# Performance work log

Hardware: AMD Instinct MI355X
Metric: run time of the kernel (lower is better)

Reference implementation:

```python
import jax, jax.numpy as jnp
import numpy as np

T, X_D, M_N, CHUNK, REDUCE = 2048, 2048, 64, 64, 8
M_D = X_D // REDUCE          # 256
DECAY_D = M_D // 4           # 64
H_D = X_D * 2                # factor=2
FF_D = 256 * round(int(H_D * (2.0 / 3.0)) / 256)  # 2816


def setup_inputs() -> dict:
    key = jax.random.key(0)
    ks = jax.random.split(key, 20)
    def lin(k, out_d, in_d):
        return (jax.random.normal(k, (out_d, in_d), jnp.float32) / np.sqrt(in_d).astype(np.float32))
    return {
        "xs": jax.random.normal(ks[0], (T, X_D), jnp.float32),
        "attn_q": lin(ks[1], X_D // REDUCE, X_D),
        "attn_k": lin(ks[2], X_D // REDUCE, X_D // REDUCE),
        "attn_v": lin(ks[3], X_D, X_D),
        "attn_o": lin(ks[4], X_D, X_D),
        "attn_r": lin(ks[5], X_D, X_D),
        "mem_f": lin(ks[6], M_N, X_D),
        "mem_q": lin(ks[7], M_D, X_D),
        "mem_k": lin(ks[8], M_D, M_D),
        "mem_v": lin(ks[9], M_D, X_D),
        "mem_o": lin(ks[10], X_D, M_D),
        "mem_r": lin(ks[11], X_D, X_D),
        "mem_beta": -jnp.ones((M_N, M_D), jnp.float32),
        "mem_decay": 3.0 * jnp.ones((M_N, DECAY_D), jnp.float32),
        "mem_l": jax.random.uniform(ks[12], (M_N, M_D), dtype=jnp.float32),
        "ff_in1": lin(ks[13], FF_D, X_D),
        "ff_in2": lin(ks[14], FF_D, X_D),
        "ff_out": lin(ks[15], X_D, FF_D),
        "sn1_g": jnp.sqrt(jnp.float32(X_D)),
        "sn2_g": jnp.sqrt(jnp.float32(X_D)),
    }


def _rotate_half(x):
    x1 = x[..., ::2]
    x2 = x[..., 1::2]
    return jnp.stack((-x2, x1), axis=-1).reshape(x.shape)


def _scale_norm(x, g):
    return x * (g / (jnp.linalg.norm(x, axis=-1, keepdims=True) + 1e-8))


def _attn(xs, Wq, Wk, Wv, Wo, Wr):
    n = CHUNK
    q = xs @ Wq.T                       # (T, dk)
    k = q @ Wk.T                        # k is computed from q (as in source)
    v = xs @ Wv.T                       # (T, x_d)
    c = xs.shape[0] // n
    dk = q.shape[-1]
    q = q.reshape(c, n, dk)
    k = k.reshape(c, n, dk)
    v = v.reshape(c, n, v.shape[-1])

    def with_prev(a):                   # prepend previous chunk (zero for chunk 0)
        prev = jnp.concatenate([jnp.zeros_like(a[:1]), a[:-1]], axis=0)
        return jnp.concatenate([prev, a], axis=1)   # (c, 2n, d)

    k2, v2 = with_prev(k), with_prev(v)

    # RoPE over 2n key positions; queries take the last n positions
    inv_freq = 1.0 / (10000.0 ** (jnp.arange(0, dk, 2, dtype=jnp.float32) / dk))
    ang = jnp.arange(2 * n, dtype=jnp.float32)[:, None] * inv_freq[None, :]
    sin = jnp.repeat(jnp.sin(ang), 2, axis=-1)      # (2n, dk) interleaved
    cos = jnp.repeat(jnp.cos(ang), 2, axis=-1)
    q = q * cos[None, n:] + _rotate_half(q) * sin[None, n:]
    k2 = k2 * cos[None] + _rotate_half(k2) * sin[None]

    qk = jnp.einsum('cnk,cmk->cnm', q, k2) / jnp.sqrt(jnp.float32(dk))
    allowed = jnp.arange(2 * n)[None, :] <= (jnp.arange(n)[:, None] + n)  # tril offset n
    A = jax.nn.softmax(jnp.where(allowed[None], qk, -jnp.inf), axis=-1)
    y = jnp.einsum('cnm,cmv->cnv', A, v2).reshape(xs.shape[0], -1)
    return (y @ Wo.T) * jax.nn.sigmoid(xs @ Wr.T)


def _mem(xs, Wf, Wq, Wk, Wv, Wo, Wr, beta_p, decay_p, l_p):
    v = xs @ Wv.T                                       # (T, m_d)
    f = jax.nn.sigmoid(xs @ Wf.T)[:, :, None]           # (T, m_n, 1)
    beta = jax.nn.sigmoid(beta_p)[None]                 # (1, m_n, m_d)
    gamma = jnp.concatenate(
        [jnp.ones((M_N, M_D - DECAY_D), xs.dtype), jax.nn.sigmoid(decay_p)], axis=1
    )[None]                                             # (1, m_n, m_d)
    ws = (1.0 - f * beta) * gamma                       # (T, m_n, m_d)
    fvs = f * v[:, None, :]                             # (T, m_n, m_d)

    def bin_assoc(ei, ej):
        ai, bi = ei
        aj, bj = ej
        return (aj * ai, aj * bi + bj)

    _, mems = jax.lax.associative_scan(bin_assoc, (ws, fvs), axis=0)  # (T, m_n, m_d)

    q = xs @ Wq.T                                       # (T, m_d)
    k = jnp.einsum('nmd,kd->nmk', mems, Wk) + l_p[None]
    A = jax.nn.softmax(jnp.einsum('nmk,nk->nm', k, q) / jnp.sqrt(jnp.float32(M_D)), axis=-1)
    y = jnp.einsum('nm,nmd->nd', A, mems)
    return (y @ Wo.T) * jax.nn.sigmoid(xs @ Wr.T)


def _ff(xs, W1, W2, Wo):
    return (jax.nn.silu(xs @ W1.T) * (xs @ W2.T)) @ Wo.T


def reference(xs, attn_q, attn_k, attn_v, attn_o, attn_r,
              mem_f, mem_q, mem_k, mem_v, mem_o, mem_r,
              mem_beta, mem_decay, mem_l,
              ff_in1, ff_in2, ff_out, sn1_g, sn2_g):
    xn = _scale_norm(xs, sn1_g)
    xs = (_attn(xn, attn_q, attn_k, attn_v, attn_o, attn_r)
          + _mem(xn, mem_f, mem_q, mem_k, mem_v, mem_o, mem_r, mem_beta, mem_decay, mem_l)
          + xs)
    xs = _ff(_scale_norm(xs, sn2_g), ff_in1, ff_in2, ff_out) + xs
    return xs
```

## Files before the change

kernel.cpp:

```cpp
#include <hip/hip_runtime.h>
#include <math.h>


typedef short bhalf8 __attribute__((ext_vector_type(8)));
typedef float f32x4 __attribute__((ext_vector_type(4)));

#define CC_LD 7168
#define COL_V   0
#define COL_B1  2048
#define COL_B2  4096
#define COL_QB  6144
#define COL_VM  6400
#define COL_QM  6656
#define COL_FG  6912

#define AS1 __attribute__((address_space(1)))
#define AS3 __attribute__((address_space(3)))

__device__ __forceinline__ float sigmoidf_(float x){ return 1.0f/(1.0f+expf(-x)); }

__device__ __forceinline__ unsigned short f2b(float f){
  unsigned u = __float_as_uint(f);
  unsigned r = (u + 0x7fffu + ((u>>16)&1u)) >> 16;
  return (unsigned short)r;
}
__device__ __forceinline__ float b2f(unsigned short h){
  return __uint_as_float(((unsigned)h)<<16);
}

__global__ void k_f2b_all(
    const float* __restrict__ av, const float* __restrict__ ar, const float* __restrict__ mr,
    const float* __restrict__ aq, const float* __restrict__ mv, const float* __restrict__ mq,
    const float* __restrict__ mf, const float* __restrict__ ao, const float* __restrict__ mo,
    const float* __restrict__ f1, const float* __restrict__ f2, const float* __restrict__ fo,
    const float* __restrict__ ak,
    unsigned short* __restrict__ WCAT, unsigned short* __restrict__ AOB,
    unsigned short* __restrict__ MOB, unsigned short* __restrict__ FFW,
    unsigned short* __restrict__ FFOB, unsigned short* __restrict__ AKB){
  int i = blockIdx.x*256 + threadIdx.x;
  const float* s; unsigned short* d; int off;
  if (i < 3571712){
    d = WCAT + (size_t)i*4;
    if      (i < 1048576){ s = av; off = i; }
    else if (i < 2097152){ s = ar; off = i-1048576; }
    else if (i < 3145728){ s = mr; off = i-2097152; }
    else if (i < 3276800){ s = aq; off = i-3145728; }
    else if (i < 3407872){ s = mv; off = i-3276800; }
    else if (i < 3538944){ s = mq; off = i-3407872; }
    else                 { s = mf; off = i-3538944; }
  }
  else if (i < 4620288){ off = i-3571712; s = ao; d = AOB  + (size_t)off*4; }
  else if (i < 4751360){ off = i-4620288; s = mo; d = MOB  + (size_t)off*4; }
  else if (i < 6193152){ off = i-4751360; s = f1;
    int row = off >> 9, c4 = off & 511;
    d = FFW + ((size_t)row*2)*2048 + c4*4; }
  else if (i < 7634944){ off = i-6193152; s = f2;
    int row = off >> 9, c4 = off & 511;
    d = FFW + ((size_t)row*2 + 1)*2048 + c4*4; }
  else if (i < 9076736){ off = i-7634944; s = fo; d = FFOB + (size_t)off*4; }
  else if (i < 9093120){ off = i-9076736; s = ak; d = AKB  + (size_t)off*4; }
  else return;
  float4 v = ((const float4*)s)[off];
  ushort4 o;
  o.x = f2b(v.x); o.y = f2b(v.y); o.z = f2b(v.z); o.w = f2b(v.w);
  *(ushort4*)d = o;
}

__global__ void k_f2bT(const float* __restrict__ s, unsigned short* __restrict__ d){
  int i = blockIdx.x, j = threadIdx.x;
  d[(size_t)j*256 + i] = f2b(s[(size_t)i*256 + j]);
}

__global__ void k_trig(float2* __restrict__ TR){
  int idx = blockIdx.x*256 + threadIdx.x;
  int pos = idx >> 7, j = idx & 127;
  float inv = powf(10000.f, -(float)j/128.f);
  float a = (float)pos * inv;
  TR[idx] = make_float2(cosf(a), sinf(a));
}

__global__ __launch_bounds__(256) void k_scalenorm_b(const float* __restrict__ x,
    const float* __restrict__ g, unsigned short* __restrict__ ob){
  int row = blockIdx.x, tid = threadIdx.x;
  const float* xr = x + (size_t)row*2048;
  float ss = 0.f;
  for (int j = tid; j < 2048; j += 256){ float v = xr[j]; ss += v*v; }
  __shared__ float red[256];
  red[tid] = ss; __syncthreads();
  for (int s = 128; s > 0; s >>= 1){ if (tid < s) red[tid] += red[tid+s]; __syncthreads(); }
  float scale = g[0] / (sqrtf(red[0]) + 1e-8f);
  unsigned short* orow = ob + (size_t)row*2048;
  for (int j4 = tid; j4 < 512; j4 += 256){
    float4 v = *(const float4*)(xr + j4*4);
    ushort4 o;
    o.x = f2b(v.x*scale); o.y = f2b(v.y*scale); o.z = f2b(v.z*scale); o.w = f2b(v.w*scale);
    ((ushort4*)orow)[j4] = o;
  }
}

__global__ __launch_bounds__(256) void k_gemm_p(
    const unsigned short* __restrict__ A, int lda,
    const unsigned short* __restrict__ B,
    float* __restrict__ C, unsigned short* __restrict__ Cb,
    int N, int K, int ldc, int epi,
    const float* __restrict__ add,
    const unsigned short* __restrict__ gate, int gate_ld,
    const unsigned short* A2, const unsigned short* B2, float* C2){
  __shared__ unsigned short LDSu[24576];
  int tid = threadIdx.x;
  int w = tid >> 6, l = tid & 63;
  int bi = blockIdx.y, bj = blockIdx.x;
  const unsigned short* Ap = A; const unsigned short* Bp = B; float* Cp = C;
  if (blockIdx.z){ Ap = A2; Bp = B2; Cp = C2; }
  int m0 = bi*128, n0 = bj*128;
  int wr = w >> 1, wc = w & 1;

  f32x4 acc[4][4];
#pragma unroll
  for (int i=0;i<4;++i)
#pragma unroll
    for (int j=0;j<4;++j){ f32x4 z = {0.f,0.f,0.f,0.f}; acc[i][j] = z; }

  const int r0 = tid >> 2;
  const int gsrc8 = (((tid&3) ^ ((tid>>3)&3)) * 8);

  auto stage = [&](int bs, int kt){
    unsigned short* db = LDSu + bs*8192;
    const unsigned short* ap0 = Ap + (size_t)(m0 + r0)*lda      + kt*32 + gsrc8;
    const unsigned short* ap1 = Ap + (size_t)(m0 + 64 + r0)*lda + kt*32 + gsrc8;
    const unsigned short* bp0 = Bp + (size_t)(n0 + r0)*K        + kt*32 + gsrc8;
    const unsigned short* bp1 = Bp + (size_t)(n0 + 64 + r0)*K   + kt*32 + gsrc8;
    __builtin_amdgcn_global_load_lds((const AS1 void*)ap0, (AS3 void*)(db + tid*8),        16, 0, 0);
    __builtin_amdgcn_global_load_lds((const AS1 void*)ap1, (AS3 void*)(db + 2048 + tid*8), 16, 0, 0);
    __builtin_amdgcn_global_load_lds((const AS1 void*)bp0, (AS3 void*)(db + 4096 + tid*8), 16, 0, 0);
    __builtin_amdgcn_global_load_lds((const AS1 void*)bp1, (AS3 void*)(db + 6144 + tid*8), 16, 0, 0);
  };

  const int nt = K >> 5;
  stage(0, 0);
  stage(1, 1);
  asm volatile("s_waitcnt vmcnt(4)" ::: "memory");
  __builtin_amdgcn_s_barrier();

  const int lr = l & 15;
  const int gsw = (((l>>4) ^ ((l>>1)&3)) * 8);
  const int aoff = (wr*64 + lr)*32 + gsw;
  const int boff = 4096 + (wc*64 + lr)*32 + gsw;

  int cur = 0;
  for (int t = 0; t < nt; ++t){
    if (t + 2 < nt) stage((t+2)%3, t+2);
    const unsigned short* Tb = LDSu + cur*8192;
    bhalf8 af[4], bfr[4];
#pragma unroll
    for (int m=0;m<4;++m) af[m]  = *(const bhalf8*)(Tb + aoff + m*512);
#pragma unroll
    for (int n=0;n<4;++n) bfr[n] = *(const bhalf8*)(Tb + boff + n*512);
    __builtin_amdgcn_s_setprio(1);
#pragma unroll
    for (int m=0;m<4;++m)
#pragma unroll
      for (int n=0;n<4;++n)
        acc[m][n] = __builtin_amdgcn_mfma_f32_16x16x32_bf16(af[m], bfr[n], acc[m][n], 0, 0, 0);
    __builtin_amdgcn_s_setprio(0);
    if (t + 1 < nt){
      if (t + 2 < nt){ asm volatile("s_waitcnt vmcnt(4)" ::: "memory"); }
      else           { asm volatile("s_waitcnt vmcnt(0)" ::: "memory"); }
      __builtin_amdgcn_s_barrier();
      cur = (cur == 2) ? 0 : cur + 1;
    }
  }

#pragma unroll
  for (int m=0;m<4;++m){
    int rowb = m0 + wr*64 + m*16 + ((l>>4)<<2);
#pragma unroll
    for (int r=0;r<4;++r){
      int row = rowb + r;
      size_t rbase = (size_t)row*ldc;
      size_t gbase = (size_t)row*gate_ld;
#pragma unroll
      for (int n=0;n<4;++n){
        int col = n0 + wc*64 + n*16 + (l&15);
        float v = acc[m][n][r];
        if (add) v += add[rbase + col];
        if (epi == 2) v *= sigmoidf_(b2f(gate[gbase + col]));
        if (epi == 3) Cb[rbase + col] = f2b(v);
        else          Cp[rbase + col] = v;
      }
    }
  }
}

__global__ __launch_bounds__(256) void k_gemm_silu(
    const unsigned short* __restrict__ A, int lda,
    const unsigned short* __restrict__ B,
    unsigned short* __restrict__ Cb, int K, int out_ld){
  __shared__ unsigned short LDSu[24576];
  int tid = threadIdx.x;
  int w = tid >> 6, l = tid & 63;
  int bi = blockIdx.y, bj = blockIdx.x;
  int m0 = bi*128, n0 = bj*128;
  int wr = w >> 1, wc = w & 1;

  f32x4 acc[4][4];
#pragma unroll
  for (int i=0;i<4;++i)
#pragma unroll
    for (int j=0;j<4;++j){ f32x4 z = {0.f,0.f,0.f,0.f}; acc[i][j] = z; }

  const int r0 = tid >> 2;
  const int gsrc8 = (((tid&3) ^ ((tid>>3)&3)) * 8);

  auto stage = [&](int bs, int kt){
    unsigned short* db = LDSu + bs*8192;
    const unsigned short* ap0 = A + (size_t)(m0 + r0)*lda      + kt*32 + gsrc8;
    const unsigned short* ap1 = A + (size_t)(m0 + 64 + r0)*lda + kt*32 + gsrc8;
    const unsigned short* bp0 = B + (size_t)(n0 + r0)*K        + kt*32 + gsrc8;
    const unsigned short* bp1 = B + (size_t)(n0 + 64 + r0)*K   + kt*32 + gsrc8;
    __builtin_amdgcn_global_load_lds((const AS1 void*)ap0, (AS3 void*)(db + tid*8),        16, 0, 0);
    __builtin_amdgcn_global_load_lds((const AS1 void*)ap1, (AS3 void*)(db + 2048 + tid*8), 16, 0, 0);
    __builtin_amdgcn_global_load_lds((const AS1 void*)bp0, (AS3 void*)(db + 4096 + tid*8), 16, 0, 0);
    __builtin_amdgcn_global_load_lds((const AS1 void*)bp1, (AS3 void*)(db + 6144 + tid*8), 16, 0, 0);
  };

  const int nt = K >> 5;
  stage(0, 0);
  stage(1, 1);
  asm volatile("s_waitcnt vmcnt(4)" ::: "memory");
  __builtin_amdgcn_s_barrier();

  const int lr = l & 15;
  const int gsw = (((l>>4) ^ ((l>>1)&3)) * 8);
  const int aoff = (wr*64 + lr)*32 + gsw;
  const int boff = 4096 + (wc*64 + lr)*32 + gsw;

  int cur = 0;
  for (int t = 0; t < nt; ++t){
    if (t + 2 < nt) stage((t+2)%3, t+2);
    const unsigned short* Tb = LDSu + cur*8192;
    bhalf8 af[4], bfr[4];
#pragma unroll
    for (int m=0;m<4;++m) af[m]  = *(const bhalf8*)(Tb + aoff + m*512);
#pragma unroll
    for (int n=0;n<4;++n) bfr[n] = *(const bhalf8*)(Tb + boff + n*512);
    __builtin_amdgcn_s_setprio(1);
#pragma unroll
    for (int m=0;m<4;++m)
#pragma unroll
      for (int n=0;n<4;++n)
        acc[m][n] = __builtin_amdgcn_mfma_f32_16x16x32_bf16(af[m], bfr[n], acc[m][n], 0, 0, 0);
    __builtin_amdgcn_s_setprio(0);
    if (t + 1 < nt){
      if (t + 2 < nt){ asm volatile("s_waitcnt vmcnt(4)" ::: "memory"); }
      else           { asm volatile("s_waitcnt vmcnt(0)" ::: "memory"); }
      __builtin_amdgcn_s_barrier();
      cur = (cur == 2) ? 0 : cur + 1;
    }
  }

#pragma unroll
  for (int m=0;m<4;++m){
    int rowb = m0 + wr*64 + m*16 + ((l>>4)<<2);
#pragma unroll
    for (int r=0;r<4;++r){
      int row = rowb + r;
      size_t gbase = (size_t)row*out_ld;
#pragma unroll
      for (int n=0;n<4;++n){
        int col = n0 + wc*64 + n*16 + (l&15);
        float v = acc[m][n][r];
        float o = __shfl_xor(v, 1);
        if ((l & 1) == 0)
          Cb[gbase + (col>>1)] = f2b(v*sigmoidf_(v)*o);
      }
    }
  }
}

__global__ __launch_bounds__(256) void k_gemm_fuse2(
    const unsigned short* __restrict__ A,  const unsigned short* __restrict__ B,
    const unsigned short* __restrict__ A2, const unsigned short* __restrict__ B2,
    const unsigned short* __restrict__ gate1, const unsigned short* __restrict__ gate2,
    const float* __restrict__ xs, float* __restrict__ XS2){
  __shared__ unsigned short LDSu[24576];
  int tid = threadIdx.x;
  int w = tid >> 6, l = tid & 63;
  int bi = blockIdx.y, bj = blockIdx.x;
  int m0 = bi*128, n0 = bj*128;
  int wr = w >> 1, wc = w & 1;

  f32x4 acc[4][4], acc2[4][4];
#pragma unroll
  for (int i=0;i<4;++i)
#pragma unroll
    for (int j=0;j<4;++j){ f32x4 z = {0.f,0.f,0.f,0.f}; acc[i][j] = z; acc2[i][j] = z; }

  const int r0 = tid >> 2;
  const int gsrc8 = (((tid&3) ^ ((tid>>3)&3)) * 8);

  auto stage = [&](int bs, int kt, const unsigned short* Ap, int lda,
                   const unsigned short* Bp, int ldb){
    unsigned short* db = LDSu + bs*8192;
    const unsigned short* ap0 = Ap + (size_t)(m0 + r0)*lda      + kt*32 + gsrc8;
    const unsigned short* ap1 = Ap + (size_t)(m0 + 64 + r0)*lda + kt*32 + gsrc8;
    const unsigned short* bp0 = Bp + (size_t)(n0 + r0)*ldb      + kt*32 + gsrc8;
    const unsigned short* bp1 = Bp + (size_t)(n0 + 64 + r0)*ldb + kt*32 + gsrc8;
    __builtin_amdgcn_global_load_lds((const AS1 void*)ap0, (AS3 void*)(db + tid*8),        16, 0, 0);
    __builtin_amdgcn_global_load_lds((const AS1 void*)ap1, (AS3 void*)(db + 2048 + tid*8), 16, 0, 0);
    __builtin_amdgcn_global_load_lds((const AS1 void*)bp0, (AS3 void*)(db + 4096 + tid*8), 16, 0, 0);
    __builtin_amdgcn_global_load_lds((const AS1 void*)bp1, (AS3 void*)(db + 6144 + tid*8), 16, 0, 0);
  };

  const int lr = l & 15;
  const int gsw = (((l>>4) ^ ((l>>1)&3)) * 8);
  const int aoff = (wr*64 + lr)*32 + gsw;
  const int boff = 4096 + (wc*64 + lr)*32 + gsw;

  {
    const int nt = 64;
    stage(0, 0, A, 2048, B, 2048);
    stage(1, 1, A, 2048, B, 2048);
    asm volatile("s_waitcnt vmcnt(4)" ::: "memory");
    __builtin_amdgcn_s_barrier();
    int cur = 0;
    for (int t = 0; t < nt; ++t){
      if (t + 2 < nt) stage((t+2)%3, t+2, A, 2048, B, 2048);
      const unsigned short* Tb = LDSu + cur*8192;
      bhalf8 af[4], bfr[4];
#pragma unroll
      for (int m=0;m<4;++m) af[m]  = *(const bhalf8*)(Tb + aoff + m*512);
#pragma unroll
      for (int n=0;n<4;++n) bfr[n] = *(const bhalf8*)(Tb + boff + n*512);
      __builtin_amdgcn_s_setprio(1);
#pragma unroll
      for (int m=0;m<4;++m)
#pragma unroll
        for (int n=0;n<4;++n)
          acc[m][n] = __builtin_amdgcn_mfma_f32_16x16x32_bf16(af[m], bfr[n], acc[m][n], 0, 0, 0);
      __builtin_amdgcn_s_setprio(0);
      if (t + 1 < nt){
        if (t + 2 < nt){ asm volatile("s_waitcnt vmcnt(4)" ::: "memory"); }
        else           { asm volatile("s_waitcnt vmcnt(0)" ::: "memory"); }
        __builtin_amdgcn_s_barrier();
        cur = (cur == 2) ? 0 : cur + 1;
      }
    }
  }
  __syncthreads();

  {
    const int nt = 8;
    stage(0, 0, A2, 256, B2, 256);
    stage(1, 1, A2, 256, B2, 256);
    asm volatile("s_waitcnt vmcnt(4)" ::: "memory");
    __builtin_amdgcn_s_barrier();
    int cur = 0;
    for (int t = 0; t < nt; ++t){
      if (t + 2 < nt) stage((t+2)%3, t+2, A2, 256, B2, 256);
      const unsigned short* Tb = LDSu + cur*8192;
      bhalf8 af[4], bfr[4];
#pragma unroll
      for (int m=0;m<4;++m) af[m]  = *(const bhalf8*)(Tb + aoff + m*512);
#pragma unroll
      for (int n=0;n<4;++n) bfr[n] = *(const bhalf8*)(Tb + boff + n*512);
      __builtin_amdgcn_s_setprio(1);
#pragma unroll
      for (int m=0;m<4;++m)
#pragma unroll
        for (int n=0;n<4;++n)
          acc2[m][n] = __builtin_amdgcn_mfma_f32_16x16x32_bf16(af[m], bfr[n], acc2[m][n], 0, 0, 0);
      __builtin_amdgcn_s_setprio(0);
      if (t + 1 < nt){
        if (t + 2 < nt){ asm volatile("s_waitcnt vmcnt(4)" ::: "memory"); }
        else           { asm volatile("s_waitcnt vmcnt(0)" ::: "memory"); }
        __builtin_amdgcn_s_barrier();
        cur = (cur == 2) ? 0 : cur + 1;
      }
    }
  }

#pragma unroll
  for (int m=0;m<4;++m){
    int rowb = m0 + wr*64 + m*16 + ((l>>4)<<2);
#pragma unroll
    for (int r=0;r<4;++r){
      int row = rowb + r;
      size_t gb = (size_t)row*CC_LD;
      size_t rb = (size_t)row*2048;
#pragma unroll
      for (int n=0;n<4;++n){
        int col = n0 + wc*64 + n*16 + (l&15);
        float v = acc[m][n][r]*sigmoidf_(b2f(gate1[gb + col]))
                + acc2[m][n][r]*sigmoidf_(b2f(gate2[gb + col]))
                + xs[rb + col];
        XS2[rb + col] = v;
      }
    }
  }
}

__global__ __launch_bounds__(256) void k_attn_scores_mfma(
    const unsigned short* __restrict__ CCqb, const float* __restrict__ K0,
    const float2* __restrict__ TR, unsigned short* __restrict__ P){
  __shared__ unsigned short Ks[128*256];
  int c = blockIdx.x, tid = threadIdx.x;
  for (int it = 0; it < 16; ++it){
    int id = tid + it*256;
    int m = id >> 5;
    int cs = (id & 31) * 8;
    float v[8];
    if (c == 0 && m < 64){
#pragma unroll
      for (int u=0;u<8;++u) v[u] = 0.f;
    } else {
      int gr = (c-1)*64 + m;
      const float* kr = K0 + (size_t)gr*256 + cs;
      float4 x0 = *(const float4*)kr, x1 = *(const float4*)(kr+4);
      v[0]=x0.x; v[1]=x0.y; v[2]=x0.z; v[3]=x0.w;
      v[4]=x1.x; v[5]=x1.y; v[6]=x1.z; v[7]=x1.w;
#pragma unroll
      for (int p2=0;p2<4;++p2){
        float2 t = TR[m*128 + (cs>>1) + p2];
        float e = v[2*p2], o = v[2*p2+1];
        v[2*p2]   = e*t.x - o*t.y;
        v[2*p2+1] = o*t.x + e*t.y;
      }
    }
    unsigned short pk[8];
#pragma unroll
    for (int u=0;u<8;++u) pk[u] = f2b(v[u]);
    int byte = m*512 + ((cs*2) ^ ((m&7)<<4));
    *(bhalf8*)((char*)&Ks[0] + byte) = *(const bhalf8*)pk;
  }
  __syncthreads();

  int w = tid >> 6, l = tid & 63;
  int lr = l & 15, lkg = l >> 4;
  f32x4 acc[8];
#pragma unroll
  for (int n=0;n<8;++n){ f32x4 z = {0.f,0.f,0.f,0.f}; acc[n] = z; }

  int iq = w*16 + lr;
  const unsigned short* qbase = CCqb + (size_t)(c*64 + iq)*CC_LD;
  int pos = 64 + iq;

  for (int kt = 0; kt < 8; ++kt){
    int k0c = kt*32 + lkg*8;
    bhalf8 q8 = *(const bhalf8*)(qbase + k0c);
    float v[8];
#pragma unroll
    for (int u=0;u<8;++u) v[u] = b2f((unsigned short)(((short*)&q8)[u]));
#pragma unroll
    for (int p2=0;p2<4;++p2){
      float2 t = TR[pos*128 + (k0c>>1) + p2];
      float e = v[2*p2], o = v[2*p2+1];
      v[2*p2]   = e*t.x - o*t.y;
      v[2*p2+1] = o*t.x + e*t.y;
    }
    unsigned short pk[8];
#pragma unroll
    for (int u=0;u<8;++u) pk[u] = f2b(v[u]);
    bhalf8 af = *(const bhalf8*)pk;
#pragma unroll
    for (int n=0;n<8;++n){
      int m = n*16 + lr;
      int byte = m*512 + ((k0c*2) ^ ((m&7)<<4));
      bhalf8 bf = *(const bhalf8*)((const char*)&Ks[0] + byte);
      acc[n] = __builtin_amdgcn_mfma_f32_16x16x32_bf16(af, bf, acc[n], 0, 0, 0);
    }
  }

  int i0 = w*16 + lkg*4;
  float mx[4] = {-1e30f,-1e30f,-1e30f,-1e30f};
  float sm[4] = {0.f,0.f,0.f,0.f};
#pragma unroll
  for (int n=0;n<8;++n){
    int col = n*16 + lr;
#pragma unroll
    for (int r=0;r<4;++r){
      float vv = acc[n][r] * (1.f/16.f);
      if (col > i0 + r + 64) vv = -1e30f;
      acc[n][r] = vv;
      mx[r] = fmaxf(mx[r], vv);
    }
  }
#pragma unroll
  for (int s=1; s<16; s<<=1)
#pragma unroll
    for (int r=0;r<4;++r) mx[r] = fmaxf(mx[r], __shfl_xor(mx[r], s));
#pragma unroll
  for (int n=0;n<8;++n)
#pragma unroll
    for (int r=0;r<4;++r){
      float e = expf(acc[n][r] - mx[r]);
      acc[n][r] = e; sm[r] += e;
    }
#pragma unroll
  for (int s=1; s<16; s<<=1)
#pragma unroll
    for (int r=0;r<4;++r) sm[r] += __shfl_xor(sm[r], s);
  float rcp[4];
#pragma unroll
  for (int r=0;r<4;++r) rcp[r] = 1.f/sm[r];

  unsigned short* Pr = P + (size_t)c*8192;
#pragma unroll
  for (int n=0;n<8;++n){
    int col = n*16 + lr;
#pragma unroll
    for (int r=0;r<4;++r)
      Pr[(i0+r)*128 + col] = f2b(acc[n][r]*rcp[r]);
  }
}

__global__ __launch_bounds__(256) void k_attn_pv_mfma(
    const unsigned short* __restrict__ P, const unsigned short* __restrict__ Vb, int vld,
    unsigned short* __restrict__ Y){
  __shared__ unsigned short Vt[128*128];
  int ct = blockIdx.x, c = blockIdx.y, tid = threadIdx.x;
  {
    int k = tid >> 1;
    int ch = (tid & 1) * 64;
    if (c == 0 && k < 64){
      for (int u=0; u<64; ++u){
        int col = ch + u;
        int byte = col*256 + ((k*2) ^ ((col&7)<<4));
        *(unsigned short*)((char*)&Vt[0] + byte) = 0;
      }
    } else {
      int gr = (c-1)*64 + k;
      const unsigned short* vr = Vb + (size_t)gr*vld + ct*128 + ch;
      for (int u8=0; u8<8; ++u8){
        bhalf8 x = *(const bhalf8*)(vr + u8*8);
#pragma unroll
        for (int u=0;u<8;++u){
          int col = ch + u8*8 + u;
          int byte = col*256 + ((k*2) ^ ((col&7)<<4));
          *(unsigned short*)((char*)&Vt[0] + byte) = (unsigned short)(((short*)&x)[u]);
        }
      }
    }
  }
  __syncthreads();
  int w = tid >> 6, l = tid & 63, lr = l & 15, lkg = l >> 4;
  f32x4 acc[8];
#pragma unroll
  for (int n=0;n<8;++n){ f32x4 z = {0.f,0.f,0.f,0.f}; acc[n] = z; }
  const unsigned short* Pr = P + (size_t)c*8192;
  for (int kt=0; kt<4; ++kt){
    int kb = kt*32 + lkg*8;
    bhalf8 af = *(const bhalf8*)(Pr + (w*16 + lr)*128 + kb);
#pragma unroll
    for (int n=0;n<8;++n){
      int col = n*16 + lr;
      int byte = col*256 + ((kb*2) ^ ((col&7)<<4));
      bhalf8 bf = *(const bhalf8*)((const char*)&Vt[0] + byte);
      acc[n] = __builtin_amdgcn_mfma_f32_16x16x32_bf16(af, bf, acc[n], 0, 0, 0);
    }
  }
  int row0 = c*64 + w*16 + lkg*4;
#pragma unroll
  for (int n=0;n<8;++n){
    int col = ct*128 + n*16 + lr;
#pragma unroll
    for (int r=0;r<4;++r)
      Y[(size_t)(row0+r)*2048 + col] = f2b(acc[n][r]);
  }
}

__global__ __launch_bounds__(256) void k_scan1(const unsigned short* __restrict__ CC,
    const float* __restrict__ beta_p, const float* __restrict__ decay_p,
    float* __restrict__ CP, float* __restrict__ CQ){
  int c = blockIdx.x, mg = blockIdx.y, d = threadIdx.x;
  __shared__ float Fs[512];
  for (int v = threadIdx.x; v < 512; v += 256){
    int s = v >> 3, j = v & 7;
    Fs[v] = sigmoidf_(b2f(CC[(size_t)(c*64+s)*CC_LD + COL_FG + mg*8 + j]));
  }
  __syncthreads();
  float beta[8], gamma[8], Pa[8], Qa[8];
#pragma unroll
  for (int j=0;j<8;++j){
    int m = mg*8+j;
    beta[j]  = sigmoidf_(beta_p[m*256+d]);
    gamma[j] = (d < 192) ? 1.f : sigmoidf_(decay_p[m*64 + (d-192)]);
    Pa[j] = 1.f; Qa[j] = 0.f;
  }
  for (int s = 0; s < 64; ++s){
    float vm = b2f(CC[(size_t)(c*64+s)*CC_LD + COL_VM + d]);
#pragma unroll
    for (int j=0;j<8;++j){
      float f = Fs[s*8+j];
      float w = (1.f - f*beta[j])*gamma[j];
      Pa[j] *= w;
      Qa[j] = w*Qa[j] + f*vm;
    }
  }
#pragma unroll
  for (int j=0;j<8;++j){
    size_t idx = ((size_t)c*64 + mg*8 + j)*256 + d;
    CP[idx] = Pa[j]; CQ[idx] = Qa[j];
  }
}

__global__ __launch_bounds__(256) void k_scan2(const float* __restrict__ CP,
    const float* __restrict__ CQ, float* __restrict__ SIN){
  int m = blockIdx.x, d = threadIdx.x;
  float S = 0.f;
  for (int c = 0; c < 32; ++c){
    size_t idx = ((size_t)c*64 + m)*256 + d;
    SIN[idx] = S;
    S = CP[idx]*S + CQ[idx];
  }
}

__global__ __launch_bounds__(256) void k_scan3(const unsigned short* __restrict__ CC,
    const float* __restrict__ beta_p, const float* __restrict__ decay_p,
    const float* __restrict__ SIN, unsigned short* __restrict__ MEMS){
  int c = blockIdx.x, mg = blockIdx.y, d = threadIdx.x;
  __shared__ float Fs[512];
  for (int v = threadIdx.x; v < 512; v += 256){
    int s = v >> 3, j = v & 7;
    Fs[v] = sigmoidf_(b2f(CC[(size_t)(c*64+s)*CC_LD + COL_FG + mg*8 + j]));
  }
  __syncthreads();
  float beta[8], gamma[8], S[8];
#pragma unroll
  for (int j=0;j<8;++j){
    int m = mg*8+j;
    beta[j]  = sigmoidf_(beta_p[m*256+d]);
    gamma[j] = (d < 192) ? 1.f : sigmoidf_(decay_p[m*64 + (d-192)]);
    S[j] = SIN[((size_t)c*64 + m)*256 + d];
  }
  for (int s = 0; s < 64; ++s){
    float vm = b2f(CC[(size_t)(c*64+s)*CC_LD + COL_VM + d]);
    size_t tb = (size_t)(c*64+s)*64;
#pragma unroll
    for (int j=0;j<8;++j){
      float f = Fs[s*8+j];
      float w = (1.f - f*beta[j])*gamma[j];
      S[j] = w*S[j] + f*vm;
      MEMS[(tb + mg*8 + j)*256 + d] = f2b(S[j]);
    }
  }
}

__global__ __launch_bounds__(256) void k_memread(const unsigned short* __restrict__ MEMS,
    const float* __restrict__ QH, const unsigned short* __restrict__ QMs, int qm_ld,
    const float* __restrict__ L, unsigned short* __restrict__ YMb){
  int t = blockIdx.x, tid = threadIdx.x;
  int wave = tid >> 6, lane = tid & 63;
  __shared__ float anorm[64];
  const unsigned short* Mt = MEMS + (size_t)t*16384;
  float4 qh4 = *(const float4*)(QH + (size_t)t*256 + lane*4);
  ushort4 qmu = *(const ushort4*)(QMs + (size_t)t*qm_ld + lane*4);
  float qm0 = b2f(qmu.x), qm1 = b2f(qmu.y), qm2 = b2f(qmu.z), qm3 = b2f(qmu.w);
  for (int mi = 0; mi < 16; ++mi){
    int m = wave*16 + mi;
    ushort4 su = *(const ushort4*)(Mt + m*256 + lane*4);
    float4 l4 = *(const float4*)(L + (size_t)m*256 + lane*4);
    float p = b2f(su.x)*qh4.x + b2f(su.y)*qh4.y + b2f(su.z)*qh4.z + b2f(su.w)*qh4.w
            + l4.x*qm0 + l4.y*qm1 + l4.z*qm2 + l4.w*qm3;
#pragma unroll
    for (int off = 32; off > 0; off >>= 1) p += __shfl_down(p, off);
    if (lane == 0) anorm[m] = p * (1.f/16.f);
  }
  __syncthreads();
  if (tid < 64){
    float v = anorm[tid];
    float mx = v;
#pragma unroll
    for (int off = 32; off > 0; off >>= 1) mx = fmaxf(mx, __shfl_xor(mx, off));
    float e = expf(v - mx);
    float s = e;
#pragma unroll
    for (int off = 32; off > 0; off >>= 1) s += __shfl_xor(s, off);
    anorm[tid] = e / s;
  }
  __syncthreads();
  float acc = 0.f;
  for (int m = 0; m < 64; ++m) acc += anorm[m]*b2f(Mt[m*256 + tid]);
  YMb[(size_t)t*256 + tid] = f2b(acc);
}

extern "C" void kernel_launch(void* const* d_in, const int* in_sizes, int n_in,
                              void* d_out, int out_size, void* d_ws, size_t ws_size,
                              hipStream_t stream){
  const float* xs        = (const float*)d_in[0];
  const float* attn_q    = (const float*)d_in[1];
  const float* attn_k    = (const float*)d_in[2];
  const float* attn_v    = (const float*)d_in[3];
  const float* attn_o    = (const float*)d_in[4];
  const float* attn_r    = (const float*)d_in[5];
  const float* mem_f     = (const float*)d_in[6];
  const float* mem_q     = (const float*)d_in[7];
  const float* mem_k     = (const float*)d_in[8];
  const float* mem_v     = (const float*)d_in[9];
  const float* mem_o     = (const float*)d_in[10];
  const float* mem_r     = (const float*)d_in[11];
  const float* mem_beta  = (const float*)d_in[12];
  const float* mem_decay = (const float*)d_in[13];
  const float* mem_l     = (const float*)d_in[14];
  const float* ff1       = (const float*)d_in[15];
  const float* ff2       = (const float*)d_in[16];
  const float* ffo       = (const float*)d_in[17];
  const float* sn1       = (const float*)d_in[18];
  const float* sn2       = (const float*)d_in[19];
  float* out = (float*)d_out;
  float* W = (float*)d_ws;

  unsigned short* XNb  = (unsigned short*)(W + 0);
  unsigned short* WCAT = (unsigned short*)(W + 2097152);
  unsigned short* CCb  = (unsigned short*)(W + 9437184);
  unsigned short* AOB  = (unsigned short*)(W + 16777216);
  unsigned short* MOB  = (unsigned short*)(W + 18874368);
  unsigned short* FFW  = (unsigned short*)(W + 19136512);
  unsigned short* FFOB = (unsigned short*)(W + 24903680);
  unsigned short* AKB  = (unsigned short*)(W + 27787264);
  unsigned short* MKTB = (unsigned short*)(W + 27820032);
  unsigned short* Ybb  = (unsigned short*)(W + 27852800);
  float*          XS2  = W + 34144256;
  unsigned short* MEMSb= (unsigned short*)(W + 38338560);
  float*          CP   = W + 55115776;
  float*          CQ   = W + 55640064;
  float*          SIN  = W + 56164352;
  float2*         TRIG = (float2*)(W + 0);
  float*          K0   = W + 32768;
  unsigned short* P    = (unsigned short*)(W + 557056);
  float*          QH   = W + 688128;
  unsigned short* YMb  = (unsigned short*)(W + 1212416);
  unsigned short* XN2b = MEMSb;
  unsigned short* H1b  = (unsigned short*)(W + 40435712);

  dim3 blk(256);

  k_f2b_all<<<dim3(35520), blk, 0, stream>>>(attn_v, attn_r, mem_r, attn_q, mem_v, mem_q,
      mem_f, attn_o, mem_o, ff1, ff2, ffo, attn_k, WCAT, AOB, MOB, FFW, FFOB, AKB);
  k_f2bT<<<dim3(256), blk, 0, stream>>>(mem_k, MKTB);

  k_scalenorm_b<<<dim3(2048), blk, 0, stream>>>(xs, sn1, XNb);

  k_gemm_p<<<dim3(56, 16), blk, 0, stream>>>(XNb, 2048, WCAT, nullptr, CCb, CC_LD, 2048, CC_LD, 3,
      nullptr, nullptr, 0, nullptr, nullptr, nullptr);

  k_trig<<<dim3(64), blk, 0, stream>>>(TRIG);

  k_gemm_p<<<dim3(2, 16, 2), blk, 0, stream>>>(CCb + COL_QB, CC_LD, AKB, K0, nullptr, 256, 256, 256, 0,
      nullptr, nullptr, 0, CCb + COL_QM, MKTB, QH);

  k_attn_scores_mfma<<<dim3(32), blk, 0, stream>>>(CCb + COL_QB, K0, TRIG, P);
  k_attn_pv_mfma<<<dim3(16, 32), blk, 0, stream>>>(P, CCb + COL_V, CC_LD, Ybb);

  k_scan1<<<dim3(32, 8), blk, 0, stream>>>(CCb, mem_beta, mem_decay, CP, CQ);
  k_scan2<<<dim3(64), blk, 0, stream>>>(CP, CQ, SIN);
  k_scan3<<<dim3(32, 8), blk, 0, stream>>>(CCb, mem_beta, mem_decay, SIN, MEMSb);
  k_memread<<<dim3(2048), blk, 0, stream>>>(MEMSb, QH, CCb + COL_QM, CC_LD, mem_l, YMb);

  k_gemm_fuse2<<<dim3(16, 16), blk, 0, stream>>>(Ybb, AOB, YMb, MOB,
      CCb + COL_B1, CCb + COL_B2, xs, XS2);

  k_scalenorm_b<<<dim3(2048), blk, 0, stream>>>(XS2, sn2, XN2b);

  k_gemm_silu<<<dim3(44, 16), blk, 0, stream>>>(XN2b, 2048, FFW, H1b, 2048, 2816);
  k_gemm_p<<<dim3(16, 16), blk, 0, stream>>>(H1b, 2816, FFOB, out, nullptr, 2048, 2816, 2048, 0,
      XS2, nullptr, 0, nullptr, nullptr, nullptr);
}
```

Baseline: 414.4 us.

## Merge prep kernels, shrink scan chunks, vectorize memread reduction

Folds the weight bf16 conversion, mem_k transpose, RoPE trig table and first scale-norm into one prep launch, removing three launches. The chunked memory scan moves from 32 chunks of 64 steps to 128 chunks of 16 steps. That gives 4x more blocks in scan1 and scan3 and shorter serial loops, but a 4x longer serial pass in scan2. The memread weighted sum now splits the 64 memory slots across 4 wave groups using ushort4 loads, followed by a shared-memory reduction. Workspace offsets for CP, CQ, SIN and TRIG are moved to fit the larger chunk buffers.

```diff
diff --git a/kernel.cpp b/kernel.cpp
--- a/kernel.cpp
+++ b/kernel.cpp
@@ -28,55 +28,73 @@
   return __uint_as_float(((unsigned)h)<<16);
 }
 
-__global__ void k_f2b_all(
+__global__ __launch_bounds__(256) void k_prep(
     const float* __restrict__ av, const float* __restrict__ ar, const float* __restrict__ mr,
     const float* __restrict__ aq, const float* __restrict__ mv, const float* __restrict__ mq,
     const float* __restrict__ mf, const float* __restrict__ ao, const float* __restrict__ mo,
     const float* __restrict__ f1, const float* __restrict__ f2, const float* __restrict__ fo,
-    const float* __restrict__ ak,
+    const float* __restrict__ ak, const float* __restrict__ mk,
+    const float* __restrict__ xsrc, const float* __restrict__ g1,
     unsigned short* __restrict__ WCAT, unsigned short* __restrict__ AOB,
     unsigned short* __restrict__ MOB, unsigned short* __restrict__ FFW,
-    unsigned short* __restrict__ FFOB, unsigned short* __restrict__ AKB){
-  int i = blockIdx.x*256 + threadIdx.x;
-  const float* s; unsigned short* d; int off;
-  if (i < 3571712){
-    d = WCAT + (size_t)i*4;
-    if      (i < 1048576){ s = av; off = i; }
-    else if (i < 2097152){ s = ar; off = i-1048576; }
-    else if (i < 3145728){ s = mr; off = i-2097152; }
-    else if (i < 3276800){ s = aq; off = i-3145728; }
-    else if (i < 3407872){ s = mv; off = i-3276800; }
-    else if (i < 3538944){ s = mq; off = i-3407872; }
-    else                 { s = mf; off = i-3538944; }
-  }
-  else if (i < 4620288){ off = i-3571712; s = ao; d = AOB  + (size_t)off*4; }
-  else if (i < 4751360){ off = i-4620288; s = mo; d = MOB  + (size_t)off*4; }
-  else if (i < 6193152){ off = i-4751360; s = f1;
-    int row = off >> 9, c4 = off & 511;
-    d = FFW + ((size_t)row*2)*2048 + c4*4; }
-  else if (i < 7634944){ off = i-6193152; s = f2;
-    int row = off >> 9, c4 = off & 511;
-    d = FFW + ((size_t)row*2 + 1)*2048 + c4*4; }
-  else if (i < 9076736){ off = i-7634944; s = fo; d = FFOB + (size_t)off*4; }
-  else if (i < 9093120){ off = i-9076736; s = ak; d = AKB  + (size_t)off*4; }
-  else return;
-  float4 v = ((const float4*)s)[off];
-  ushort4 o;
-  o.x = f2b(v.x); o.y = f2b(v.y); o.z = f2b(v.z); o.w = f2b(v.w);
-  *(ushort4*)d = o;
-}
-
-__global__ void k_f2bT(const float* __restrict__ s, unsigned short* __restrict__ d){
-  int i = blockIdx.x, j = threadIdx.x;
-  d[(size_t)j*256 + i] = f2b(s[(size_t)i*256 + j]);
-}
-
-__global__ void k_trig(float2* __restrict__ TR){
-  int idx = blockIdx.x*256 + threadIdx.x;
-  int pos = idx >> 7, j = idx & 127;
-  float inv = powf(10000.f, -(float)j/128.f);
-  float a = (float)pos * inv;
-  TR[idx] = make_float2(cosf(a), sinf(a));
+    unsigned short* __restrict__ FFOB, unsigned short* __restrict__ AKB,
+    unsigned short* __restrict__ MKTB, float2* __restrict__ TR,
+    unsigned short* __restrict__ XNb){
+  int bid = blockIdx.x, tid = threadIdx.x;
+  if (bid < 35520){
+    int i = bid*256 + tid;
+    const float* s; unsigned short* d; int off;
+    if (i < 3571712){
+      d = WCAT + (size_t)i*4;
+      if      (i < 1048576){ s = av; off = i; }
+      else if (i < 2097152){ s = ar; off = i-1048576; }
+      else if (i < 3145728){ s = mr; off = i-2097152; }
+      else if (i < 3276800){ s = aq; off = i-3145728; }
+      else if (i < 3407872){ s = mv; off = i-3276800; }
+      else if (i < 3538944){ s = mq; off = i-3407872; }
+      else                 { s = mf; off = i-3538944; }
+    }
+    else if (i < 4620288){ off = i-3571712; s = ao; d = AOB  + (size_t)off*4; }
+    else if (i < 4751360){ off = i-4620288; s = mo; d = MOB  + (size_t)off*4; }
+    else if (i < 6193152){ off = i-4751360; s = f1;
+      int row = off >> 9, c4 = off & 511;
+      d = FFW + ((size_t)row*2)*2048 + c4*4; }
+    else if (i < 7634944){ off = i-6193152; s = f2;
+      int row = off >> 9, c4 = off & 511;
+      d = FFW + ((size_t)row*2 + 1)*2048 + c4*4; }
+    else if (i < 9076736){ off = i-7634944; s = fo; d = FFOB + (size_t)off*4; }
+    else if (i < 9093120){ off = i-9076736; s = ak; d = AKB  + (size_t)off*4; }
+    else return;
+    float4 v = ((const float4*)s)[off];
+    ushort4 o;
+    o.x = f2b(v.x); o.y = f2b(v.y); o.z = f2b(v.z); o.w = f2b(v.w);
+    *(ushort4*)d = o;
+  } else if (bid < 35776){
+    int i = bid - 35520, j = tid;
+    MKTB[(size_t)j*256 + i] = f2b(mk[(size_t)i*256 + j]);
+  } else if (bid < 35840){
+    int idx = (bid - 35776)*256 + tid;
+    int pos = idx >> 7, j = idx & 127;
+    float inv = powf(10000.f, -(float)j/128.f);
+    float a = (float)pos * inv;
+    TR[idx] = make_float2(cosf(a), sinf(a));
+  } else {
+    int row = bid - 35840;
+    const float* xr = xsrc + (size_t)row*2048;
+    float ss = 0.f;
+    for (int j = tid; j < 2048; j += 256){ float v = xr[j]; ss += v*v; }
+    __shared__ float red[256];
+    red[tid] = ss; __syncthreads();
+    for (int s = 128; s > 0; s >>= 1){ if (tid < s) red[tid] += red[tid+s]; __syncthreads(); }
+    float scale = g1[0] / (sqrtf(red[0]) + 1e-8f);
+    unsigned short* orow = XNb + (size_t)row*2048;
+    for (int j4 = tid; j4 < 512; j4 += 256){
+      float4 v = *(const float4*)(xr + j4*4);
+      ushort4 o;
+      o.x = f2b(v.x*scale); o.y = f2b(v.y*scale); o.z = f2b(v.z*scale); o.w = f2b(v.w*scale);
+      ((ushort4*)orow)[j4] = o;
+    }
+  }
 }
 
 __global__ __launch_bounds__(256) void k_scalenorm_b(const float* __restrict__ x,
@@ -573,10 +591,10 @@
     const float* __restrict__ beta_p, const float* __restrict__ decay_p,
     float* __restrict__ CP, float* __restrict__ CQ){
   int c = blockIdx.x, mg = blockIdx.y, d = threadIdx.x;
-  __shared__ float Fs[512];
-  for (int v = threadIdx.x; v < 512; v += 256){
-    int s = v >> 3, j = v & 7;
-    Fs[v] = sigmoidf_(b2f(CC[(size_t)(c*64+s)*CC_LD + COL_FG + mg*8 + j]));
+  __shared__ float Fs[128];
+  if (threadIdx.x < 128){
+    int s = threadIdx.x >> 3, j = threadIdx.x & 7;
+    Fs[threadIdx.x] = sigmoidf_(b2f(CC[(size_t)(c*16+s)*CC_LD + COL_FG + mg*8 + j]));
   }
   __syncthreads();
   float beta[8], gamma[8], Pa[8], Qa[8];
@@ -587,8 +605,8 @@
     gamma[j] = (d < 192) ? 1.f : sigmoidf_(decay_p[m*64 + (d-192)]);
     Pa[j] = 1.f; Qa[j] = 0.f;
   }
-  for (int s = 0; s < 64; ++s){
-    float vm = b2f(CC[(size_t)(c*64+s)*CC_LD + COL_VM + d]);
+  for (int s = 0; s < 16; ++s){
+    float vm = b2f(CC[(size_t)(c*16+s)*CC_LD + COL_VM + d]);
 #pragma unroll
     for (int j=0;j<8;++j){
       float f = Fs[s*8+j];
@@ -608,7 +626,7 @@
     const float* __restrict__ CQ, float* __restrict__ SIN){
   int m = blockIdx.x, d = threadIdx.x;
   float S = 0.f;
-  for (int c = 0; c < 32; ++c){
+  for (int c = 0; c < 128; ++c){
     size_t idx = ((size_t)c*64 + m)*256 + d;
     SIN[idx] = S;
     S = CP[idx]*S + CQ[idx];
@@ -619,10 +637,10 @@
     const float* __restrict__ beta_p, const float* __restrict__ decay_p,
     const float* __restrict__ SIN, unsigned short* __restrict__ MEMS){
   int c = blockIdx.x, mg = blockIdx.y, d = threadIdx.x;
-  __shared__ float Fs[512];
-  for (int v = threadIdx.x; v < 512; v += 256){
-    int s = v >> 3, j = v & 7;
-    Fs[v] = sigmoidf_(b2f(CC[(size_t)(c*64+s)*CC_LD + COL_FG + mg*8 + j]));
+  __shared__ float Fs[128];
+  if (threadIdx.x < 128){
+    int s = threadIdx.x >> 3, j = threadIdx.x & 7;
+    Fs[threadIdx.x] = sigmoidf_(b2f(CC[(size_t)(c*16+s)*CC_LD + COL_FG + mg*8 + j]));
   }
   __syncthreads();
   float beta[8], gamma[8], S[8];
@@ -633,9 +651,9 @@
     gamma[j] = (d < 192) ? 1.f : sigmoidf_(decay_p[m*64 + (d-192)]);
     S[j] = SIN[((size_t)c*64 + m)*256 + d];
   }
-  for (int s = 0; s < 64; ++s){
-    float vm = b2f(CC[(size_t)(c*64+s)*CC_LD + COL_VM + d]);
-    size_t tb = (size_t)(c*64+s)*64;
+  for (int s = 0; s < 16; ++s){
+    float vm = b2f(CC[(size_t)(c*16+s)*CC_LD + COL_VM + d]);
+    size_t tb = (size_t)(c*16+s)*64;
 #pragma unroll
     for (int j=0;j<8;++j){
       float f = Fs[s*8+j];
@@ -652,6 +670,7 @@
   int t = blockIdx.x, tid = threadIdx.x;
   int wave = tid >> 6, lane = tid & 63;
   __shared__ float anorm[64];
+  __shared__ float red2[4][64][4];
   const unsigned short* Mt = MEMS + (size_t)t*16384;
   float4 qh4 = *(const float4*)(QH + (size_t)t*256 + lane*4);
   ushort4 qmu = *(const ushort4*)(QMs + (size_t)t*qm_ld + lane*4);
@@ -679,9 +698,29 @@
     anorm[tid] = e / s;
   }
   __syncthreads();
-  float acc = 0.f;
-  for (int m = 0; m < 64; ++m) acc += anorm[m]*b2f(Mt[m*256 + tid]);
-  YMb[(size_t)t*256 + tid] = f2b(acc);
+  int mq = tid >> 6, dq = tid & 63;
+  float a0=0.f, a1=0.f, a2=0.f, a3=0.f;
+#pragma unroll
+  for (int mi = 0; mi < 16; ++mi){
+    int m = mq*16 + mi;
+    ushort4 su = *(const ushort4*)(Mt + m*256 + dq*4);
+    float wgt = anorm[m];
+    a0 += wgt*b2f(su.x); a1 += wgt*b2f(su.y);
+    a2 += wgt*b2f(su.z); a3 += wgt*b2f(su.w);
+  }
+  red2[mq][dq][0]=a0; red2[mq][dq][1]=a1; red2[mq][dq][2]=a2; red2[mq][dq][3]=a3;
+  __syncthreads();
+  if (tid < 64){
+    float r0=0.f, r1=0.f, r2=0.f, r3=0.f;
+#pragma unroll
+    for (int g=0; g<4; ++g){
+      r0 += red2[g][tid][0]; r1 += red2[g][tid][1];
+      r2 += red2[g][tid][2]; r3 += red2[g][tid][3];
+    }
+    ushort4 o;
+    o.x = f2b(r0); o.y = f2b(r1); o.z = f2b(r2); o.w = f2b(r3);
+    *(ushort4*)(YMb + (size_t)t*256 + tid*4) = o;
+  }
 }
 
 extern "C" void kernel_launch(void* const* d_in, const int* in_sizes, int n_in,
@@ -723,9 +762,9 @@
   float*          XS2  = W + 34144256;
   unsigned short* MEMSb= (unsigned short*)(W + 38338560);
   float*          CP   = W + 55115776;
-  float*          CQ   = W + 55640064;
-  float*          SIN  = W + 56164352;
-  float2*         TRIG = (float2*)(W + 0);
+  float*          CQ   = W + 57212928;
+  float*          SIN  = W + 59310080;
+  float2*         TRIG = (float2*)(W + 61407232);
   float*          K0   = W + 32768;
   unsigned short* P    = (unsigned short*)(W + 557056);
   float*          QH   = W + 688128;
@@ -735,26 +774,22 @@
 
   dim3 blk(256);
 
-  k_f2b_all<<<dim3(35520), blk, 0, stream>>>(attn_v, attn_r, mem_r, attn_q, mem_v, mem_q,
-      mem_f, attn_o, mem_o, ff1, ff2, ffo, attn_k, WCAT, AOB, MOB, FFW, FFOB, AKB);
-  k_f2bT<<<dim3(256), blk, 0, stream>>>(mem_k, MKTB);
-
-  k_scalenorm_b<<<dim3(2048), blk, 0, stream>>>(xs, sn1, XNb);
+  k_prep<<<dim3(37888), blk, 0, stream>>>(attn_v, attn_r, mem_r, attn_q, mem_v, mem_q,
+      mem_f, attn_o, mem_o, ff1, ff2, ffo, attn_k, mem_k, xs, sn1,
+      WCAT, AOB, MOB, FFW, FFOB, AKB, MKTB, TRIG, XNb);
 
   k_gemm_p<<<dim3(56, 16), blk, 0, stream>>>(XNb, 2048, WCAT, nullptr, CCb, CC_LD, 2048, CC_LD, 3,
       nullptr, nullptr, 0, nullptr, nullptr, nullptr);
 
-  k_trig<<<dim3(64), blk, 0, stream>>>(TRIG);
-
   k_gemm_p<<<dim3(2, 16, 2), blk, 0, stream>>>(CCb + COL_QB, CC_LD, AKB, K0, nullptr, 256, 256, 256, 0,
       nullptr, nullptr, 0, CCb + COL_QM, MKTB, QH);
 
   k_attn_scores_mfma<<<dim3(32), blk, 0, stream>>>(CCb + COL_QB, K0, TRIG, P);
   k_attn_pv_mfma<<<dim3(16, 32), blk, 0, stream>>>(P, CCb + COL_V, CC_LD, Ybb);
 
-  k_scan1<<<dim3(32, 8), blk, 0, stream>>>(CCb, mem_beta, mem_decay, CP, CQ);
+  k_scan1<<<dim3(128, 8), blk, 0, stream>>>(CCb, mem_beta, mem_decay, CP, CQ);
   k_scan2<<<dim3(64), blk, 0, stream>>>(CP, CQ, SIN);
-  k_scan3<<<dim3(32, 8), blk, 0, stream>>>(CCb, mem_beta, mem_decay, SIN, MEMSb);
+  k_scan3<<<dim3(128, 8), blk, 0, stream>>>(CCb, mem_beta, mem_decay, SIN, MEMSb);
   k_memread<<<dim3(2048), blk, 0, stream>>>(MEMSb, QH, CCb + COL_QM, CC_LD, mem_l, YMb);
 
   k_gemm_fuse2<<<dim3(16, 16), blk, 0, stream>>>(Ybb, AOB, YMb, MOB,
```

Measured after the change: 412.1 us. No clear change (-0.5%).
